# Performance work log

Hardware: AMD Instinct MI355X
Metric: run time of the kernel (lower is better)

## Reference

```python
import jax, jax.numpy as jnp
import numpy as np

LN_EPS = 1e-5  # torch nn.LayerNorm default


def setup_inputs() -> dict:
    key = jax.random.key(0)
    kx, kw = jax.random.split(key)
    T, B, D = 1024, 8, 2048
    x = jax.random.normal(kx, (T, B, D), dtype=jnp.float32)
    c0 = jnp.zeros((B, D), dtype=jnp.float32)
    # Linear(n_embd, 3*n_embd, bias=False) weight: [3D, D], scaled for sane activations
    W = jax.random.normal(kw, (3 * D, D), dtype=jnp.float32) / np.sqrt(D)
    gamma = jnp.ones((D,), dtype=jnp.float32)
    beta = jnp.zeros((D,), dtype=jnp.float32)
    return {"x": x, "c0": c0, "W": W, "gamma": gamma, "beta": beta}


def reference(x, c0, W, gamma, beta):
    # x: [T, B, D], c0: [B, D], W: [3D, D]
    T, B, D = x.shape
    # Projection for all timesteps at once (same math as per-step Linear).
    ufr = jnp.einsum('tbd,ed->tbe', x, W)  # [T, B, 3D]
    u, f, r = jnp.split(ufr, 3, axis=-1)
    f = jax.nn.sigmoid(f)
    r = jax.nn.sigmoid(r)

    def step(c_prev, inp):
        x_t, u_t, f_t, r_t = inp
        c_t = f_t * c_prev + (1.0 - f_t) * u_t
        h_t = r_t * jnp.tanh(c_t) + (1.0 - r_t) * x_t
        return c_t, h_t

    c_T, h = jax.lax.scan(step, c0, (x, u, f, r))  # h: [T, B, D]

    g = jax.nn.gelu(h, approximate=False)  # torch F.gelu default = exact erf
    mean = jnp.mean(g, axis=-1, keepdims=True)
    var = jnp.var(g, axis=-1, keepdims=True)
    out = (g - mean) * jax.lax.rsqrt(var + LN_EPS) * gamma + beta
    return out, c_T
```

## Files before the change

### kernel.cpp

```cpp
#include <hip/hip_runtime.h>
#include <hip/hip_bf16.h>

#define T_DIM 1024
#define B_DIM 8
#define D_DIM 2048
#define E_DIM 6144
#define N_ROWS 8192
#define K_DIM 2048
#define LN_EPS 1e-5f

#define S2  128
#define CH2 8
#define BD (B_DIM * D_DIM)

typedef short bf16x8 __attribute__((ext_vector_type(8)));
typedef float f32x4 __attribute__((ext_vector_type(4)));

__device__ __forceinline__ unsigned short f2bf(float f) {
  unsigned u = __float_as_uint(f);
  u += 0x7fffu + ((u >> 16) & 1u);
  return (unsigned short)(u >> 16);
}
__device__ __forceinline__ float bf2f(unsigned short h) {
  return __uint_as_float(((unsigned)h) << 16);
}
__device__ __forceinline__ float fast_sigmoid(float x) {
  return __builtin_amdgcn_rcpf(1.f + __expf(-x));
}
__device__ __forceinline__ float fast_tanh(float x) {
  return 1.f - 2.f * __builtin_amdgcn_rcpf(__expf(2.f * x) + 1.f);
}

__global__ __launch_bounds__(256) void cvt2_kernel(
    const float* __restrict__ src0, unsigned short* __restrict__ dst0, int n0,
    const float* __restrict__ src1, unsigned short* __restrict__ dst1, int n1) {
  int i = blockIdx.x * 256 + threadIdx.x;
  const float* s;
  unsigned short* d;
  if (i < n0) {
    s = src0; d = dst0;
  } else {
    i -= n0;
    if (i >= n1) return;
    s = src1; d = dst1;
  }
  float4 v = reinterpret_cast<const float4*>(s)[i];
  ushort4 o;
  o.x = f2bf(v.x); o.y = f2bf(v.y); o.z = f2bf(v.z); o.w = f2bf(v.w);
  reinterpret_cast<ushort4*>(d)[i] = o;
}

#define NT2 32

__global__ __launch_bounds__(512, 2) void gemm8_kernel(
    const unsigned short* __restrict__ A,
    const unsigned short* __restrict__ Bw,
    unsigned short* __restrict__ C) {
  extern __shared__ __align__(16) char smem[];
  const int tid  = threadIdx.x;
  const int lane = tid & 63;
  const int wave = tid >> 6;
  const int wm = wave >> 2;
  const int wn = wave & 3;

  const int bid = blockIdx.x;
  const int tileM = ((bid & 7) * 4 + ((bid >> 3) & 3)) * 256;
  const int tileN = (bid >> 5) * 256;

  const int p0i = wave * 2048 + lane * 16;
  const int p1i = p0i + 1024;
  const int q0i = p0i ^ (((p0i >> 9) & 1) << 5);
  const int q1i = p1i ^ (((p1i >> 9) & 1) << 5);
  const int go0 = ((q0i >> 6) & 127) * 4096 + ((q0i >> 13) << 6) + (q0i & 63);
  const int go1 = ((q1i >> 6) & 127) * 4096 + ((q1i >> 13) << 6) + (q1i & 63);
  const char* Ab = (const char*)A + (size_t)tileM * 4096;
  const char* Bb = (const char*)Bw + (size_t)tileN * 4096;

#define STAGE(kt, h, bufOff)                                                 \
  {                                                                          \
    const char* gs_ = ((h) < 2 ? Ab : Bb) +                                  \
                      (size_t)(((h) & 1) * 128) * 4096 + (size_t)(kt) * 128; \
    char* ds_ = smem + (bufOff) + (h) * 16384 + wave * 2048;                 \
    __builtin_amdgcn_global_load_lds(                                        \
        (const __attribute__((address_space(1))) void*)(gs_ + go0),          \
        (__attribute__((address_space(3))) void*)ds_, 16, 0, 0);             \
    __builtin_amdgcn_global_load_lds(                                        \
        (const __attribute__((address_space(1))) void*)(gs_ + go1),          \
        (__attribute__((address_space(3))) void*)(ds_ + 1024), 16, 0, 0);    \
  }

  const int xbit = ((lane >> 3) & 1) << 5;
  const int aBase = wm * 16384 +
                    (((lane & 15) * 64 + (lane >> 4) * 16) ^ xbit);
  const int bBase = 32768 + (wn >> 1) * 16384 +
                    ((((wn & 1) * 64 + (lane & 15)) * 64 + (lane >> 4) * 16) ^ xbit);

#define RDA(m, bufOff)                                                          \
  a[m][0] = *reinterpret_cast<const bf16x8*>(smem + (bufOff) + aBase + (m) * 1024);        \
  a[m][1] = *reinterpret_cast<const bf16x8*>(smem + (bufOff) + aBase + (m) * 1024 + 8192);
#define RDB(n, bufOff)                                                          \
  b[n][0] = *reinterpret_cast<const bf16x8*>(smem + (bufOff) + bBase + (n) * 1024);        \
  b[n][1] = *reinterpret_cast<const bf16x8*>(smem + (bufOff) + bBase + (n) * 1024 + 8192);
#define MM(m, n)                                                                \
  acc[m][n] = __builtin_amdgcn_mfma_f32_16x16x32_bf16(a[m][0], b[n][0], acc[m][n], 0, 0, 0); \
  acc[m][n] = __builtin_amdgcn_mfma_f32_16x16x32_bf16(a[m][1], b[n][1], acc[m][n], 0, 0, 0);

  bf16x8 a[8][2], b[4][2];
  f32x4 acc[8][4] = {};

  STAGE(0, 0, 0); STAGE(0, 1, 0); STAGE(0, 2, 0); STAGE(0, 3, 0);
  STAGE(1, 0, 65536); STAGE(1, 1, 65536);
  asm volatile("s_waitcnt vmcnt(4)" ::: "memory");
  __builtin_amdgcn_s_barrier();
  RDA(0, 0); RDA(1, 0); RDA(2, 0); RDA(3, 0);
  RDB(0, 0); RDB(1, 0);

  for (int j = 0; j < NT2; ++j) {
    const int buf  = (j & 1) << 16;
    const int nbuf = buf ^ 65536;
    asm volatile("s_waitcnt lgkmcnt(0)" ::: "memory");
    __builtin_amdgcn_s_setprio(1);
    if (j < NT2 - 1) STAGE(j + 1, 2, nbuf);
    RDA(4, buf); RDA(5, buf); RDA(6, buf); RDA(7, buf);
    MM(0, 0); MM(0, 1); MM(1, 0); MM(1, 1);
    MM(2, 0); MM(2, 1); MM(3, 0); MM(3, 1);
    __builtin_amdgcn_s_setprio(0);
    __builtin_amdgcn_s_barrier();
    asm volatile("s_waitcnt lgkmcnt(0)" ::: "memory");
    __builtin_amdgcn_s_setprio(1);
    if (j < NT2 - 1) STAGE(j + 1, 3, nbuf);
    RDB(2, buf); RDB(3, buf);
    MM(4, 0); MM(4, 1); MM(5, 0); MM(5, 1);
    MM(6, 0); MM(6, 1); MM(7, 0); MM(7, 1);
    __builtin_amdgcn_s_setprio(0);
    __builtin_amdgcn_s_barrier();
    asm volatile("s_waitcnt lgkmcnt(0)" ::: "memory");
    __builtin_amdgcn_s_setprio(1);
    if (j < NT2 - 2) STAGE(j + 2, 0, buf);
    MM(0, 2); MM(0, 3); MM(1, 2); MM(1, 3);
    MM(2, 2); MM(2, 3); MM(3, 2); MM(3, 3);
    __builtin_amdgcn_s_setprio(0);
    __builtin_amdgcn_s_barrier();
    if (j < NT2 - 2) {
      STAGE(j + 2, 1, buf);
      asm volatile("s_waitcnt vmcnt(4)" ::: "memory");
    } else if (j == NT2 - 2) {
      asm volatile("s_waitcnt vmcnt(0)" ::: "memory");
    }
    __builtin_amdgcn_s_barrier();
    __builtin_amdgcn_s_setprio(1);
    RDA(0, nbuf); RDA(1, nbuf); RDA(2, nbuf); RDA(3, nbuf);
    RDB(0, nbuf); RDB(1, nbuf);
    MM(4, 2); MM(4, 3); MM(5, 2); MM(5, 3);
    MM(6, 2); MM(6, 3); MM(7, 2); MM(7, 3);
    __builtin_amdgcn_s_setprio(0);
    __builtin_amdgcn_s_barrier();
  }

  const int crow = (lane >> 4) * 4;
  const int ccol = lane & 15;
#pragma unroll
  for (int m = 0; m < 8; ++m) {
#pragma unroll
    for (int n = 0; n < 4; ++n) {
#pragma unroll
      for (int jj = 0; jj < 4; ++jj) {
        int row = tileM + wm * 128 + m * 16 + crow + jj;
        int col = tileN + wn * 64 + n * 16 + ccol;
        C[(size_t)row * E_DIM + col] = f2bf(acc[m][n][jj]);
      }
    }
  }
#undef STAGE
#undef RDA
#undef RDB
#undef MM
}

__global__ __launch_bounds__(256) void scan_p1_kernel(
    const unsigned short* __restrict__ ufr,
    float* __restrict__ Aout, float* __restrict__ Bout) {
  const int idx = blockIdx.x * 256 + threadIdx.x;
  const int s = blockIdx.y;
  const int b = idx >> 11;
  const int d = idx & 2047;
  const unsigned short* up =
      ufr + ((size_t)(s * CH2) * B_DIM + b) * E_DIM + d;
  float Aacc = 1.f, Bacc = 0.f;
#pragma unroll
  for (int it = 0; it < CH2; ++it) {
    float u  = bf2f(up[0]);
    float fl = bf2f(up[D_DIM]);
    float f = fast_sigmoid(fl);
    Aacc *= f;
    Bacc = f * Bacc + (1.f - f) * u;
    up += (size_t)B_DIM * E_DIM;
  }
  Aout[(size_t)s * BD + idx] = Aacc;
  Bout[(size_t)s * BD + idx] = Bacc;
}

__global__ __launch_bounds__(256) void scan_p2_kernel(
    const float* __restrict__ c0,
    const float* __restrict__ Ain, const float* __restrict__ Bin,
    float* __restrict__ cs, float* __restrict__ cT) {
  const int idx = blockIdx.x * 256 + threadIdx.x;
  float c = c0[idx];
  for (int s = 0; s < S2; ++s) {
    cs[(size_t)s * BD + idx] = c;
    c = Ain[(size_t)s * BD + idx] * c + Bin[(size_t)s * BD + idx];
  }
  cT[idx] = c;
}

__global__ __launch_bounds__(256) void scan_p3ln_kernel(
    const unsigned short* __restrict__ xb,
    const unsigned short* __restrict__ ufr,
    const float* __restrict__ cs,
    const float* __restrict__ gamma,
    const float* __restrict__ beta,
    float* __restrict__ out) {
  const int b = blockIdx.x & (B_DIM - 1);
  const int s = blockIdx.x >> 3;
  const int tid = threadIdx.x;
  const int lane = tid & 63;
  const int wave = tid >> 6;
  const int d0 = tid * 8;
  __shared__ float red[8];

  float c[8];
  {
    const float* csp = cs + (size_t)s * BD + b * D_DIM + d0;
    float4 v0 = *(const float4*)csp;
    float4 v1 = *(const float4*)(csp + 4);
    c[0]=v0.x; c[1]=v0.y; c[2]=v0.z; c[3]=v0.w;
    c[4]=v1.x; c[5]=v1.y; c[6]=v1.z; c[7]=v1.w;
  }
  float gam[8], bet[8];
  {
    float4 g0 = *(const float4*)(gamma + d0);
    float4 g1 = *(const float4*)(gamma + d0 + 4);
    float4 b0 = *(const float4*)(beta + d0);
    float4 b1 = *(const float4*)(beta + d0 + 4);
    gam[0]=g0.x; gam[1]=g0.y; gam[2]=g0.z; gam[3]=g0.w;
    gam[4]=g1.x; gam[5]=g1.y; gam[6]=g1.z; gam[7]=g1.w;
    bet[0]=b0.x; bet[1]=b0.y; bet[2]=b0.z; bet[3]=b0.w;
    bet[4]=b1.x; bet[5]=b1.y; bet[6]=b1.z; bet[7]=b1.w;
  }

  for (int it = 0; it < CH2; ++it) {
    const size_t rowo = (size_t)(s * CH2 + it) * B_DIM + b;
    const unsigned short* up = ufr + rowo * E_DIM + d0;
    const unsigned short* xp = xb + rowo * D_DIM + d0;
    ushort4 uv0 = *(const ushort4*)up;
    ushort4 uv1 = *(const ushort4*)(up + 4);
    ushort4 fv0 = *(const ushort4*)(up + D_DIM);
    ushort4 fv1 = *(const ushort4*)(up + D_DIM + 4);
    ushort4 rv0 = *(const ushort4*)(up + 2 * D_DIM);
    ushort4 rv1 = *(const ushort4*)(up + 2 * D_DIM + 4);
    ushort4 xv0 = *(const ushort4*)xp;
    ushort4 xv1 = *(const ushort4*)(xp + 4);
    unsigned short uu[8] = {uv0.x, uv0.y, uv0.z, uv0.w, uv1.x, uv1.y, uv1.z, uv1.w};
    unsigned short ff[8] = {fv0.x, fv0.y, fv0.z, fv0.w, fv1.x, fv1.y, fv1.z, fv1.w};
    unsigned short rr[8] = {rv0.x, rv0.y, rv0.z, rv0.w, rv1.x, rv1.y, rv1.z, rv1.w};
    unsigned short xx[8] = {xv0.x, xv0.y, xv0.z, xv0.w, xv1.x, xv1.y, xv1.z, xv1.w};

    float g[8];
    float s1 = 0.f, sq = 0.f;
#pragma unroll
    for (int jj = 0; jj < 8; ++jj) {
      float f = fast_sigmoid(bf2f(ff[jj]));
      float r = fast_sigmoid(bf2f(rr[jj]));
      c[jj] = f * c[jj] + (1.f - f) * bf2f(uu[jj]);
      float h = r * fast_tanh(c[jj]) + (1.f - r) * bf2f(xx[jj]);
      float gg = 0.5f * h * (1.f + erff(h * 0.70710678118654752f));
      g[jj] = gg;
      s1 += gg;
      sq += gg * gg;
    }
#pragma unroll
    for (int off = 32; off; off >>= 1) {
      s1 += __shfl_xor(s1, off);
      sq += __shfl_xor(sq, off);
    }
    if (lane == 0) { red[wave] = s1; red[4 + wave] = sq; }
    __syncthreads();
    float S1 = red[0] + red[1] + red[2] + red[3];
    float Sq = red[4] + red[5] + red[6] + red[7];
    __syncthreads();
    float mean = S1 * (1.f / D_DIM);
    float var  = Sq * (1.f / D_DIM) - mean * mean;
    float inv = rsqrtf(var + LN_EPS);

    float* op = out + rowo * D_DIM + d0;
    float4 o0 = {(g[0] - mean) * inv * gam[0] + bet[0],
                 (g[1] - mean) * inv * gam[1] + bet[1],
                 (g[2] - mean) * inv * gam[2] + bet[2],
                 (g[3] - mean) * inv * gam[3] + bet[3]};
    float4 o1 = {(g[4] - mean) * inv * gam[4] + bet[4],
                 (g[5] - mean) * inv * gam[5] + bet[5],
                 (g[6] - mean) * inv * gam[6] + bet[6],
                 (g[7] - mean) * inv * gam[7] + bet[7]};
    *(float4*)op = o0;
    *(float4*)(op + 4) = o1;
  }
}

extern "C" void kernel_launch(void* const* d_in, const int* in_sizes, int n_in,
                              void* d_out, int out_size, void* d_ws, size_t ws_size,
                              hipStream_t stream) {
  const float* x     = (const float*)d_in[0];
  const float* c0    = (const float*)d_in[1];
  const float* W     = (const float*)d_in[2];
  const float* gamma = (const float*)d_in[3];
  const float* beta  = (const float*)d_in[4];
  float* out = (float*)d_out;
  float* cT  = out + (size_t)N_ROWS * D_DIM;

  unsigned short* ufr = (unsigned short*)d_ws;
  unsigned short* xb  = ufr + (size_t)N_ROWS * E_DIM;
  unsigned short* wb  = xb + (size_t)N_ROWS * K_DIM;

  float* Abuf = (float*)wb;
  float* Bbuf = Abuf + (size_t)S2 * BD;
  float* csb  = Bbuf + (size_t)S2 * BD;

  int nx4 = N_ROWS * K_DIM / 4;
  int nw4 = E_DIM * K_DIM / 4;
  cvt2_kernel<<<(nx4 + nw4 + 255) / 256, 256, 0, stream>>>(x, xb, nx4, W, wb, nw4);

  (void)hipFuncSetAttribute((const void*)gemm8_kernel,
                            hipFuncAttributeMaxDynamicSharedMemorySize, 131072);
  gemm8_kernel<<<768, 512, 131072, stream>>>(xb, wb, ufr);

  dim3 sg(BD / 256, S2);
  scan_p1_kernel<<<sg, 256, 0, stream>>>(ufr, Abuf, Bbuf);
  scan_p2_kernel<<<BD / 256, 256, 0, stream>>>(c0, Abuf, Bbuf, csb, cT);
  scan_p3ln_kernel<<<B_DIM * S2, 256, 0, stream>>>(xb, ufr, csb, gamma, beta, out);
}
```

Measured before the change: 267.6 us.

## Store scan chunk carries and states in bf16, vectorize pass 1, shrink pass-2 blocks

The chunked-scan intermediates (per-chunk A/B products and chunk-start states) are stored as bf16 instead of fp32, halving their memory traffic across the three scan kernels. Pass 1 now handles four adjacent features per thread with ushort4 loads and stores. Pass 2 uses 64-thread blocks so its 16K serial-chain threads spread over more CUs. Rounding the carried states to bf16 adds error to the recurrence, especially through the chained multiply in pass 2.

```diff
diff --git a/kernel.cpp b/kernel.cpp
--- a/kernel.cpp
+++ b/kernel.cpp
@@ -179,36 +179,45 @@
 
 __global__ __launch_bounds__(256) void scan_p1_kernel(
     const unsigned short* __restrict__ ufr,
-    float* __restrict__ Aout, float* __restrict__ Bout) {
-  const int idx = blockIdx.x * 256 + threadIdx.x;
+    unsigned short* __restrict__ Aout, unsigned short* __restrict__ Bout) {
+  const int idx4 = blockIdx.x * 256 + threadIdx.x;
   const int s = blockIdx.y;
-  const int b = idx >> 11;
-  const int d = idx & 2047;
+  const int b = idx4 >> 9;
+  const int d = (idx4 & 511) * 4;
   const unsigned short* up =
       ufr + ((size_t)(s * CH2) * B_DIM + b) * E_DIM + d;
-  float Aacc = 1.f, Bacc = 0.f;
+  float A0 = 1.f, A1 = 1.f, A2 = 1.f, A3 = 1.f;
+  float Bv0 = 0.f, Bv1 = 0.f, Bv2 = 0.f, Bv3 = 0.f;
 #pragma unroll
   for (int it = 0; it < CH2; ++it) {
-    float u  = bf2f(up[0]);
-    float fl = bf2f(up[D_DIM]);
-    float f = fast_sigmoid(fl);
-    Aacc *= f;
-    Bacc = f * Bacc + (1.f - f) * u;
+    ushort4 uv = *(const ushort4*)up;
+    ushort4 fv = *(const ushort4*)(up + D_DIM);
+    float f0 = fast_sigmoid(bf2f(fv.x));
+    float f1 = fast_sigmoid(bf2f(fv.y));
+    float f2 = fast_sigmoid(bf2f(fv.z));
+    float f3 = fast_sigmoid(bf2f(fv.w));
+    A0 *= f0; Bv0 = f0 * Bv0 + (1.f - f0) * bf2f(uv.x);
+    A1 *= f1; Bv1 = f1 * Bv1 + (1.f - f1) * bf2f(uv.y);
+    A2 *= f2; Bv2 = f2 * Bv2 + (1.f - f2) * bf2f(uv.z);
+    A3 *= f3; Bv3 = f3 * Bv3 + (1.f - f3) * bf2f(uv.w);
     up += (size_t)B_DIM * E_DIM;
   }
-  Aout[(size_t)s * BD + idx] = Aacc;
-  Bout[(size_t)s * BD + idx] = Bacc;
-}
-
-__global__ __launch_bounds__(256) void scan_p2_kernel(
+  size_t o = (size_t)s * BD + b * D_DIM + d;
+  ushort4 ao = {f2bf(A0), f2bf(A1), f2bf(A2), f2bf(A3)};
+  ushort4 bo = {f2bf(Bv0), f2bf(Bv1), f2bf(Bv2), f2bf(Bv3)};
+  *(ushort4*)(Aout + o) = ao;
+  *(ushort4*)(Bout + o) = bo;
+}
+
+__global__ __launch_bounds__(64) void scan_p2_kernel(
     const float* __restrict__ c0,
-    const float* __restrict__ Ain, const float* __restrict__ Bin,
-    float* __restrict__ cs, float* __restrict__ cT) {
-  const int idx = blockIdx.x * 256 + threadIdx.x;
+    const unsigned short* __restrict__ Ain, const unsigned short* __restrict__ Bin,
+    unsigned short* __restrict__ cs, float* __restrict__ cT) {
+  const int idx = blockIdx.x * 64 + threadIdx.x;
   float c = c0[idx];
   for (int s = 0; s < S2; ++s) {
-    cs[(size_t)s * BD + idx] = c;
-    c = Ain[(size_t)s * BD + idx] * c + Bin[(size_t)s * BD + idx];
+    cs[(size_t)s * BD + idx] = f2bf(c);
+    c = bf2f(Ain[(size_t)s * BD + idx]) * c + bf2f(Bin[(size_t)s * BD + idx]);
   }
   cT[idx] = c;
 }
@@ -216,7 +225,7 @@
 __global__ __launch_bounds__(256) void scan_p3ln_kernel(
     const unsigned short* __restrict__ xb,
     const unsigned short* __restrict__ ufr,
-    const float* __restrict__ cs,
+    const unsigned short* __restrict__ csb,
     const float* __restrict__ gamma,
     const float* __restrict__ beta,
     float* __restrict__ out) {
@@ -230,11 +239,11 @@
 
   float c[8];
   {
-    const float* csp = cs + (size_t)s * BD + b * D_DIM + d0;
-    float4 v0 = *(const float4*)csp;
-    float4 v1 = *(const float4*)(csp + 4);
-    c[0]=v0.x; c[1]=v0.y; c[2]=v0.z; c[3]=v0.w;
-    c[4]=v1.x; c[5]=v1.y; c[6]=v1.z; c[7]=v1.w;
+    const unsigned short* csp = csb + (size_t)s * BD + b * D_DIM + d0;
+    ushort4 v0 = *(const ushort4*)csp;
+    ushort4 v1 = *(const ushort4*)(csp + 4);
+    c[0]=bf2f(v0.x); c[1]=bf2f(v0.y); c[2]=bf2f(v0.z); c[3]=bf2f(v0.w);
+    c[4]=bf2f(v1.x); c[5]=bf2f(v1.y); c[6]=bf2f(v1.z); c[7]=bf2f(v1.w);
   }
   float gam[8], bet[8];
   {
@@ -321,9 +330,9 @@
   unsigned short* xb  = ufr + (size_t)N_ROWS * E_DIM;
   unsigned short* wb  = xb + (size_t)N_ROWS * K_DIM;
 
-  float* Abuf = (float*)wb;
-  float* Bbuf = Abuf + (size_t)S2 * BD;
-  float* csb  = Bbuf + (size_t)S2 * BD;
+  unsigned short* Abuf = wb;
+  unsigned short* Bbuf = Abuf + (size_t)S2 * BD;
+  unsigned short* csb  = Bbuf + (size_t)S2 * BD;
 
   int nx4 = N_ROWS * K_DIM / 4;
   int nw4 = E_DIM * K_DIM / 4;
@@ -333,8 +342,8 @@
                             hipFuncAttributeMaxDynamicSharedMemorySize, 131072);
   gemm8_kernel<<<768, 512, 131072, stream>>>(xb, wb, ufr);
 
-  dim3 sg(BD / 256, S2);
+  dim3 sg(BD / 4 / 256, S2);
   scan_p1_kernel<<<sg, 256, 0, stream>>>(ufr, Abuf, Bbuf);
-  scan_p2_kernel<<<BD / 256, 256, 0, stream>>>(c0, Abuf, Bbuf, csb, cT);
+  scan_p2_kernel<<<BD / 64, 64, 0, stream>>>(c0, Abuf, Bbuf, csb, cT);
   scan_p3ln_kernel<<<B_DIM * S2, 256, 0, stream>>>(xb, ufr, csb, gamma, beta, out);
 }
```

Measured after the change: 266.9 us. About the same (-0.3%).
